# Optimization experiments

Measured on AMD Instinct MI355X. Metric: run time of the kernel, lower is better.

The kernel has to match this reference:

```python
import jax, jax.numpy as jnp
import numpy as np

# Graph / model dims (see shape_source)
N, E = 50000, 1600000          # nodes, edges
NE = 10                         # spectral supports per edge (nfreq)
NIN, NOUT1, NOUT2 = 1, 32, 16   # dataset.num_features, conv out, gate out
NIN2 = NOUT1 + NOUT2            # 48, input to layers 2/3 and fc2


def setup_inputs() -> dict:
    key = jax.random.key(0)
    ks = jax.random.split(key, 32)

    def g(k, shape, scale=0.1):
        return jax.random.normal(k, shape, dtype=jnp.float32) * scale

    inp = {
        "x": g(ks[0], (N, NIN), 1.0),
        "edge_attr": g(ks[1], (E, NE), 1.0),
        "edge_index": jax.random.randint(ks[2], (2, E), 0, N, dtype=jnp.int32),
    }
    i = 3
    for l, nin in zip((1, 2, 3), (NIN, NIN2, NIN2)):
        inp[f"W{l}"] = g(ks[i], (NE, nin, NOUT1)); i += 1   # SpectConv weight [K,in,out]
        inp[f"b{l}"] = g(ks[i], (NOUT1,)); i += 1            # SpectConv bias
        inp[f"U{l}"] = g(ks[i], (nin, NOUT2)); i += 1        # fc11 weight (in,out)
        inp[f"ub{l}"] = g(ks[i], (NOUT2,)); i += 1
        inp[f"V{l}"] = g(ks[i], (nin, NOUT2)); i += 1        # fc12 weight
        inp[f"vb{l}"] = g(ks[i], (NOUT2,)); i += 1
    inp["fc2_w"] = g(ks[i], (NIN2, 1)); i += 1
    inp["fc2_b"] = g(ks[i], (1,))
    return inp


def ml3_layer(x, src, dst, edge_attr, W, b, U, ub, V, vb):
    """ML3Layer(learnedge=False): SpectConv(selfconn=False) + gated linear branch."""
    xs = x[src]  # [E, C] gather source-node features once
    out = jnp.broadcast_to(b, (x.shape[0], W.shape[2]))
    for k in range(W.shape[0]):  # K=10 spectral supports, small fixed loop
        # message: edge_attr[:,k] * x_j ; aggregate: scatter-add at target
        h = jax.ops.segment_sum(edge_attr[:, k:k + 1] * xs, dst, num_segments=x.shape[0])
        out = out + h @ W[k]
    gate = (x @ U + ub) * (x @ V + vb)  # fc11(x) * fc12(x)
    return jnp.concatenate([jax.nn.relu(out), gate], axis=1)  # [N, 48]


def reference(x, edge_attr, W1, b1, U1, ub1, V1, vb1,
              W2, b2, U2, ub2, V2, vb2,
              W3, b3, U3, ub3, V3, vb3,
              fc2_w, fc2_b, edge_index):
    src, dst = edge_index[0], edge_index[1]  # PyG: row 0 = source j, row 1 = target i
    x = ml3_layer(x, src, dst, edge_attr, W1, b1, U1, ub1, V1, vb1)
    x = ml3_layer(x, src, dst, edge_attr, W2, b2, U2, ub2, V2, vb2)
    x = ml3_layer(x, src, dst, edge_attr, W3, b3, U3, ub3, V3, vb3)
    return x @ fc2_w + fc2_b  # [N, 1]
```

## Files before the change

kernel.cpp:

```cpp
#include <hip/hip_runtime.h>


constexpr int K  = 10;
constexpr int C1 = 32;
constexpr int C2 = 16;
constexpr int CC = 48;
constexpr int KD = 480;
constexpr int KSTEPS = 15;
constexpr int RTILE = 4096;
constexpr int RS_WAVES  = 8;
constexpr int RS_ROUNDS = RTILE / (RS_WAVES * 64);

typedef short bf16x8 __attribute__((ext_vector_type(8)));
typedef float f32x4  __attribute__((ext_vector_type(4)));
typedef unsigned int uintx4 __attribute__((ext_vector_type(4)));

static __device__ __forceinline__ unsigned short f2bf(float f) {
    unsigned int u = __float_as_uint(f);
    return (unsigned short)((u + 0x7FFFu + ((u >> 16) & 1u)) >> 16);
}
static __device__ __forceinline__ float bf2f(unsigned short h) {
    return __uint_as_float(((unsigned int)h) << 16);
}
static __device__ __forceinline__ unsigned int pk2(float a, float b) {
    return (unsigned int)f2bf(a) | ((unsigned int)f2bf(b) << 16);
}

__global__ __launch_bounds__(256)
void build_kernel(const float* __restrict__ ea, const int* __restrict__ src,
                  const int* __restrict__ dst, unsigned short* __restrict__ rec,
                  unsigned short* __restrict__ keys0, unsigned int* __restrict__ idx0,
                  int E) {
    int e = blockIdx.x * 256 + threadIdx.x;
    if (e >= E) return;
    keys0[e] = (unsigned short)dst[e];
    idx0[e] = (unsigned int)e;
    const float2* ep = (const float2*)(ea + (size_t)e * K);
    float2 a0 = ep[0], a1 = ep[1], a2 = ep[2], a3 = ep[3], a4 = ep[4];
    uint4 r0, r1;
    r0.x = pk2(a0.x, a0.y); r0.y = pk2(a1.x, a1.y);
    r0.z = pk2(a2.x, a2.y); r0.w = pk2(a3.x, a3.y);
    r1.x = pk2(a4.x, a4.y); r1.y = (unsigned int)src[e];
    r1.z = 0u; r1.w = 0u;
    uint4* rp = (uint4*)(rec + (size_t)e * 16);
    rp[0] = r0; rp[1] = r1;
}

template<int SHIFT>
__global__ __launch_bounds__(256)
void rcount_kernel(const unsigned short* __restrict__ keys,
                   unsigned int* __restrict__ counts, int E, int NB) {
    __shared__ unsigned int h[256];
    h[threadIdx.x] = 0;
    __syncthreads();
    int end = min((blockIdx.x + 1) * RTILE, E);
    for (int i = blockIdx.x * RTILE + threadIdx.x; i < end; i += 256)
        atomicAdd(&h[(keys[i] >> SHIFT) & 255], 1);
    __syncthreads();
    counts[(size_t)threadIdx.x * NB + blockIdx.x] = h[threadIdx.x];
}

__global__ __launch_bounds__(256)
void digit_scan_kernel(const unsigned int* __restrict__ counts,
                       unsigned int* __restrict__ gscan,
                       unsigned int* __restrict__ dtot, int NB) {
    __shared__ unsigned int s[256];
    int d = blockIdx.x, t = threadIdx.x;
    const unsigned int* row = counts + (size_t)d * NB;
    unsigned int* orow = gscan + (size_t)d * NB;
    unsigned int running = 0;
    for (int base = 0; base < NB; base += 256) {
        int i = base + t;
        unsigned int v = (i < NB) ? row[i] : 0u;
        s[t] = v;
        __syncthreads();
#pragma unroll
        for (int off = 1; off < 256; off <<= 1) {
            unsigned int a = (t >= off) ? s[t - off] : 0u;
            __syncthreads();
            s[t] += a;
            __syncthreads();
        }
        if (i < NB) orow[i] = running + s[t] - v;
        running += s[255];
        __syncthreads();
    }
    if (t == 0) dtot[d] = running;
}

template<int SHIFT>
__global__ __launch_bounds__(512)
void rscatter_kernel(const unsigned short* __restrict__ keyIn,
                     const unsigned int* __restrict__ idxIn,
                     const unsigned int* __restrict__ gscan,
                     const unsigned int* __restrict__ dtot,
                     unsigned short* __restrict__ keyOut,
                     unsigned int* __restrict__ idxOut, int E, int NB) {
    __shared__ unsigned int hw[RS_WAVES][256];
    __shared__ unsigned int wex[RS_WAVES][256];
    __shared__ unsigned int wrun[RS_WAVES][256];
    __shared__ unsigned int dbt[256];
    __shared__ unsigned int gb[256];
    int t = threadIdx.x, b = blockIdx.x;
    int w = t >> 6, lane = t & 63;
    {
        unsigned int* hwf = &hw[0][0];
        unsigned int* wrf = &wrun[0][0];
        for (int i = t; i < RS_WAVES * 256; i += 512) { hwf[i] = 0; wrf[i] = 0; }
    }
    unsigned int dv = (t < 256) ? dtot[t] : 0u;
    if (t < 256) dbt[t] = dv;
    __syncthreads();
#pragma unroll
    for (int off = 1; off < 256; off <<= 1) {
        unsigned int a = (t >= off && t < 256) ? dbt[t - off] : 0u;
        __syncthreads();
        if (t < 256) dbt[t] += a;
        __syncthreads();
    }
    if (t < 256) gb[t] = (dbt[t] - dv) + gscan[(size_t)t * NB + b];
    int base = b * RTILE + w * (RTILE / RS_WAVES);
    unsigned short keys[RS_ROUNDS]; unsigned int idxs[RS_ROUNDS]; unsigned int dig[RS_ROUNDS];
#pragma unroll
    for (int r = 0; r < RS_ROUNDS; ++r) {
        int i = base + r * 64 + lane;
        if (i < E) {
            keys[r] = keyIn[i];
            idxs[r] = idxIn[i];
            dig[r] = (keys[r] >> SHIFT) & 255u;
            atomicAdd(&hw[w][dig[r]], 1u);
        } else dig[r] = 0xFFFFFFFFu;
    }
    __syncthreads();
    if (t < 256) {
        unsigned int s = 0;
#pragma unroll
        for (int ww = 0; ww < RS_WAVES; ++ww) { wex[ww][t] = s; s += hw[ww][t]; }
    }
    __syncthreads();
#pragma unroll
    for (int r = 0; r < RS_ROUNDS; ++r) {
        bool valid = dig[r] != 0xFFFFFFFFu;
        unsigned int d = valid ? dig[r] : 0u;
        unsigned long long mask = __ballot(valid);
#pragma unroll
        for (int bit = 0; bit < 8; ++bit) {
            unsigned long long bb = __ballot(valid && ((d >> bit) & 1u));
            mask &= ((d >> bit) & 1u) ? bb : ~bb;
        }
        unsigned int old = 0;
        if (valid) {
            int leader = __ffsll((long long)mask) - 1;
            if (lane == leader) {
                old = wrun[w][d];
                wrun[w][d] = old + (unsigned int)__popcll(mask);
            }
            old = __shfl(old, leader);
            unsigned int myrank = (unsigned int)__popcll(mask & ((1ull << lane) - 1ull));
            unsigned int pos = gb[d] + wex[w][d] + old + myrank;
            keyOut[pos] = keys[r];
            idxOut[pos] = idxs[r];
        }
    }
}

__global__ __launch_bounds__(256)
void materialize_kernel(const unsigned int* __restrict__ idxS,
                        const unsigned short* __restrict__ rec,
                        unsigned short* __restrict__ ea_t,
                        int* __restrict__ src_d, int E, int Epad) {
    int r = blockIdx.x * 256 + threadIdx.x;
    if (r >= Epad) return;
    if (r < E) {
        unsigned int p = idxS[r];
        const uint4* rp = (const uint4*)(rec + (size_t)p * 16);
        uint4 r0 = rp[0], r1 = rp[1];
        src_d[r] = (int)r1.y;
        ea_t[(size_t)0 * Epad + r] = (unsigned short)r0.x;
        ea_t[(size_t)1 * Epad + r] = (unsigned short)(r0.x >> 16);
        ea_t[(size_t)2 * Epad + r] = (unsigned short)r0.y;
        ea_t[(size_t)3 * Epad + r] = (unsigned short)(r0.y >> 16);
        ea_t[(size_t)4 * Epad + r] = (unsigned short)r0.z;
        ea_t[(size_t)5 * Epad + r] = (unsigned short)(r0.z >> 16);
        ea_t[(size_t)6 * Epad + r] = (unsigned short)r0.w;
        ea_t[(size_t)7 * Epad + r] = (unsigned short)(r0.w >> 16);
        ea_t[(size_t)8 * Epad + r] = (unsigned short)r1.x;
        ea_t[(size_t)9 * Epad + r] = (unsigned short)(r1.x >> 16);
    } else {
        src_d[r] = 0;
#pragma unroll
        for (int k = 0; k < K; ++k) ea_t[(size_t)k * Epad + r] = 0;
    }
}

__global__ __launch_bounds__(256)
void rowptr_kernel(const unsigned short* __restrict__ keysS,
                   int* __restrict__ rowptr, int N, int E) {
    int n = blockIdx.x * 256 + threadIdx.x;
    if (n >= N) return;
    int lo = 0, hi = E;
    while (lo < hi) {
        int mid = (lo + hi) >> 1;
        if ((int)keysS[mid] < n) lo = mid + 1; else hi = mid;
    }
    rowptr[n] = lo;
}

static __device__ __forceinline__
void wconv_entry(const float* __restrict__ W, unsigned short* __restrict__ out,
                 int li, int kdact, int cin) {
    int t = li >> 7, rem = li & 127, h = rem >> 6, l = rem & 63;
    int cp = (l & 15) + 16 * h;
    int kbase = t * 32 + ((l >> 4) << 3);
    unsigned int pk[4];
#pragma unroll
    for (int q = 0; q < 4; ++q) {
        unsigned int a = 0, b = 0;
        int kd0 = kbase + 2 * q, kd1 = kd0 + 1;
        if (kd0 < kdact) { int c = kd0 / K, k = kd0 % K; a = f2bf(W[((size_t)k * cin + c) * C1 + cp]); }
        if (kd1 < kdact) { int c = kd1 / K, k = kd1 % K; b = f2bf(W[((size_t)k * cin + c) * C1 + cp]); }
        pk[q] = a | (b << 16);
    }
    uint4 u; u.x = pk[0]; u.y = pk[1]; u.z = pk[2]; u.w = pk[3];
    *(uint4*)(out + (size_t)li * 8) = u;
}

__global__ __launch_bounds__(256)
void wconv_all_kernel(const float* __restrict__ W1, const float* __restrict__ W2,
                      const float* __restrict__ W3,
                      unsigned short* __restrict__ Bfrg1,
                      unsigned short* __restrict__ Bfrag2,
                      unsigned short* __restrict__ Bfrag3) {
    int i = blockIdx.x * 256 + threadIdx.x;
    if (i < 1920)        wconv_entry(W2, Bfrag2, i, KD, CC);
    else if (i < 3840)   wconv_entry(W3, Bfrag3, i - 1920, KD, CC);
    else if (i < 3968)   wconv_entry(W1, Bfrg1, i - 3840, K, 1);
}

__global__ __launch_bounds__(256)
void gather1_kernel(const float* __restrict__ x, const unsigned short* __restrict__ ea_t,
                    const int* __restrict__ src_d, const int* __restrict__ rowptr,
                    unsigned short* __restrict__ Hb, int N, int E, int Epad) {
    int n = blockIdx.x * 4 + (int)(threadIdx.x >> 6);
    if (n >= N) return;
    int l = threadIdx.x & 63;
    int k = l & 15, g = l >> 4;
    int lo = rowptr[n], hi = (n + 1 < N) ? rowptr[n + 1] : E;
    float h = 0.f;
    for (int base = (lo & ~31); base < hi; base += 32) {
        float xs = 0.f;
        int e = base + l;
        if (l < 32 && e >= lo && e < hi) xs = x[src_d[e]];
        bf16x8 av = {0, 0, 0, 0, 0, 0, 0, 0};
        if (k < K) av = *(const bf16x8*)(ea_t + (size_t)k * Epad + base + g * 8);
        float p = 0.f;
#pragma unroll
        for (int j = 0; j < 8; ++j) {
            float xv = __shfl(xs, g * 8 + j);
            p = fmaf(bf2f((unsigned short)av[j]), xv, p);
        }
        h += p;
    }
    h += __shfl_xor(h, 16);
    h += __shfl_xor(h, 32);
    if (l < 32) Hb[(size_t)n * 32 + l] = (l < K) ? f2bf(h) : (unsigned short)0;
}

__global__ __launch_bounds__(256)
void gatherM_kernel(const unsigned short* __restrict__ xb,
                    const unsigned short* __restrict__ ea_t,
                    const int* __restrict__ src_d, const int* __restrict__ rowptr,
                    unsigned short* __restrict__ Hb, int N, int E, int Epad) {
    int n = blockIdx.x * 4 + (int)(threadIdx.x >> 6);
    if (n >= N) return;
    int l = threadIdx.x & 63;
    int lo = rowptr[n], hi = (n + 1 < N) ? rowptr[n + 1] : E;
    int row = l & 15;
    int eoff = (l >> 4) * 8;
    const unsigned short* aplane = ea_t + (size_t)row * Epad;
    f32x4 d0 = {0.f,0.f,0.f,0.f}, d1 = {0.f,0.f,0.f,0.f}, d2 = {0.f,0.f,0.f,0.f};
    for (int base = (lo & ~31); base < hi; base += 32) {
        int e0 = base + eoff;
        uintx4 afu = {0u, 0u, 0u, 0u};
        if (row < K) afu = *(const uintx4*)(aplane + e0);
        int4 sA = *(const int4*)(src_d + e0);
        int4 sB = *(const int4*)(src_d + e0 + 4);
        int s0 = sA.x, s1 = sA.y, s2 = sA.z, s3 = sA.w;
        int s4 = sB.x, s5 = sB.y, s6 = sB.z, s7 = sB.w;
        bool v0,v1,v2,v3,v4,v5,v6,v7;
#define VCK(r, sv, vv) { int e = e0 + r; vv = (e >= lo) && (e < hi); sv = vv ? sv : 0; }
        VCK(0,s0,v0) VCK(1,s1,v1) VCK(2,s2,v2) VCK(3,s3,v3)
        VCK(4,s4,v4) VCK(5,s5,v5) VCK(6,s6,v6) VCK(7,s7,v7)
#undef VCK
        afu[0] &= (v0 ? 0x0000ffffu : 0u) | (v1 ? 0xffff0000u : 0u);
        afu[1] &= (v2 ? 0x0000ffffu : 0u) | (v3 ? 0xffff0000u : 0u);
        afu[2] &= (v4 ? 0x0000ffffu : 0u) | (v5 ? 0xffff0000u : 0u);
        afu[3] &= (v6 ? 0x0000ffffu : 0u) | (v7 ? 0xffff0000u : 0u);
        bf16x8 af = __builtin_bit_cast(bf16x8, afu);
        unsigned int bw0[4], bw1[4], bw2[4];
#define GPAIR(q, sa, sb) { \
        const unsigned short* pa = xb + (size_t)sa * CC + row; \
        const unsigned short* pb = xb + (size_t)sb * CC + row; \
        bw0[q] = (unsigned int)pa[0]  | ((unsigned int)pb[0]  << 16); \
        bw1[q] = (unsigned int)pa[16] | ((unsigned int)pb[16] << 16); \
        bw2[q] = (unsigned int)pa[32] | ((unsigned int)pb[32] << 16); }
        GPAIR(0, s0, s1)
        GPAIR(1, s2, s3)
        GPAIR(2, s4, s5)
        GPAIR(3, s6, s7)
#undef GPAIR
        uintx4 u0 = {bw0[0], bw0[1], bw0[2], bw0[3]};
        uintx4 u1 = {bw1[0], bw1[1], bw1[2], bw1[3]};
        uintx4 u2 = {bw2[0], bw2[1], bw2[2], bw2[3]};
        d0 = __builtin_amdgcn_mfma_f32_16x16x32_bf16(af, __builtin_bit_cast(bf16x8, u0), d0, 0, 0, 0);
        d1 = __builtin_amdgcn_mfma_f32_16x16x32_bf16(af, __builtin_bit_cast(bf16x8, u1), d1, 0, 0, 0);
        d2 = __builtin_amdgcn_mfma_f32_16x16x32_bf16(af, __builtin_bit_cast(bf16x8, u2), d2, 0, 0, 0);
    }
    int rb = (l >> 4) * 4;
    if (rb < K) {
#define STORE_CG(dv, cg) { \
        size_t off = (size_t)n * KD + (size_t)((cg) * 16 + row) * K + rb; \
        *(unsigned int*)(Hb + off) = (unsigned int)f2bf(dv[0]) | ((unsigned int)f2bf(dv[1]) << 16); \
        if (rb != 8) \
            *(unsigned int*)(Hb + off + 2) = (unsigned int)f2bf(dv[2]) | ((unsigned int)f2bf(dv[3]) << 16); }
        STORE_CG(d0, 0) STORE_CG(d1, 1) STORE_CG(d2, 2)
#undef STORE_CG
    }
}

template<int KS>
__global__ __launch_bounds__(256)
void hgemm_kernel(const unsigned short* __restrict__ Hb,
                  const unsigned short* __restrict__ Bfrag,
                  float* __restrict__ acc, int N) {
    __shared__ unsigned short Bl[KS * 2 * 64 * 8];
    for (int i = threadIdx.x; i < KS * 2 * 64 * 4; i += 256)
        ((unsigned int*)Bl)[i] = ((const unsigned int*)Bfrag)[i];
    __syncthreads();
    int tile = blockIdx.x * 4 + (int)(threadIdx.x >> 6);
    int l = threadIdx.x & 63;
    int node0 = tile * 16;
    if (node0 >= N) return;
    constexpr int KDl = KS * 32;
    int row = l & 15, koff = (l >> 4) * 8;
    f32x4 a0 = {0.f,0.f,0.f,0.f}, a1 = {0.f,0.f,0.f,0.f};
#pragma unroll
    for (int t = 0; t < KS; ++t) {
        bf16x8 af = *(const bf16x8*)(Hb + (size_t)(node0 + row) * KDl + t * 32 + koff);
        bf16x8 b0 = *(const bf16x8*)(&Bl[(t * 2 + 0) * 64 * 8 + l * 8]);
        bf16x8 b1 = *(const bf16x8*)(&Bl[(t * 2 + 1) * 64 * 8 + l * 8]);
        a0 = __builtin_amdgcn_mfma_f32_16x16x32_bf16(af, b0, a0, 0, 0, 0);
        a1 = __builtin_amdgcn_mfma_f32_16x16x32_bf16(af, b1, a1, 0, 0, 0);
    }
    int col = l & 15, rbase = (l >> 4) * 4;
#pragma unroll
    for (int r = 0; r < 4; ++r) {
        int node = node0 + rbase + r;
        acc[(size_t)node * C1 + col]      = a0[r];
        acc[(size_t)node * C1 + 16 + col] = a1[r];
    }
}

template<int CIN, bool FINAL>
__global__ __launch_bounds__(256)
void epilogue_kernel(const float* __restrict__ acc, const float* __restrict__ b,
                     const float* __restrict__ x, const float* __restrict__ U,
                     const float* __restrict__ ub, const float* __restrict__ V,
                     const float* __restrict__ vb, float* __restrict__ xnext,
                     unsigned short* __restrict__ xbnext,
                     const float* __restrict__ fc2w, const float* __restrict__ fc2b,
                     float* __restrict__ out, int N) {
    int node = blockIdx.x * 16 + (int)(threadIdx.x >> 4);
    int cp   = threadIdx.x & 15;
    if (node >= N) return;
    float r0 = acc[(size_t)node * C1 + cp]      + b[cp];
    float r1 = acc[(size_t)node * C1 + 16 + cp] + b[16 + cp];
    r0 = r0 > 0.f ? r0 : 0.f;
    r1 = r1 > 0.f ? r1 : 0.f;
    float u = ub[cp], v = vb[cp];
#pragma unroll
    for (int c = 0; c < CIN; ++c) {
        float xc = x[(size_t)node * CIN + c];
        u = fmaf(xc, U[c * C2 + cp], u);
        v = fmaf(xc, V[c * C2 + cp], v);
    }
    float g = u * v;
    if (!FINAL) {
        xnext[(size_t)node * CC + cp]      = r0;
        xnext[(size_t)node * CC + 16 + cp] = r1;
        xnext[(size_t)node * CC + 32 + cp] = g;
        xbnext[(size_t)node * CC + cp]      = f2bf(r0);
        xbnext[(size_t)node * CC + 16 + cp] = f2bf(r1);
        xbnext[(size_t)node * CC + 32 + cp] = f2bf(g);
    } else {
        float dp = r0 * fc2w[cp] + r1 * fc2w[16 + cp] + g * fc2w[32 + cp];
#pragma unroll
        for (int off = 8; off; off >>= 1) dp += __shfl_xor(dp, off, 16);
        if (cp == 0) out[node] = dp + fc2b[0];
    }
}

__global__ __launch_bounds__(256)
void edge1_kernel(const float* __restrict__ x, const float* __restrict__ W1,
                  const float* __restrict__ ea, const int* __restrict__ src,
                  const int* __restrict__ dst, float* __restrict__ acc, int E) {
    __shared__ float Ws[K * C1];
    for (int i = threadIdx.x; i < K * C1; i += 256) Ws[i] = W1[i];
    __syncthreads();
    int gid = blockIdx.x * 256 + threadIdx.x;
    int e = gid >> 5;
    if (e >= E) return;
    int cp = threadIdx.x & 31;
    float xv = x[src[e]];
    const float* eap = ea + (size_t)e * K;
    float m = 0.f;
#pragma unroll
    for (int k = 0; k < K; ++k) m = fmaf(eap[k], Ws[k * C1 + cp], m);
    atomicAdd(acc + (size_t)dst[e] * C1 + cp, m * xv);
}

template<int CIN>
__global__ __launch_bounds__(256)
void xw_kernel(const float* __restrict__ x, const float* __restrict__ W,
               float* __restrict__ XW, int N) {
    __shared__ float Ws[K * CIN * C1];
    for (int i = threadIdx.x; i < K * CIN * C1; i += 256) Ws[i] = W[i];
    __syncthreads();
    int node = blockIdx.x * 8 + (int)(threadIdx.x >> 5);
    int cp = threadIdx.x & 31;
    if (node >= N) return;
    float xv[CIN];
#pragma unroll
    for (int c = 0; c < CIN; ++c) xv[c] = x[(size_t)node * CIN + c];
#pragma unroll
    for (int k = 0; k < K; ++k) {
        float a = 0.f;
#pragma unroll
        for (int c = 0; c < CIN; ++c) a = fmaf(xv[c], Ws[(k * CIN + c) * C1 + cp], a);
        XW[(size_t)node * (K * C1) + k * C1 + cp] = a;
    }
}

__global__ __launch_bounds__(256)
void edge_kernel(const float* __restrict__ XW, const float* __restrict__ ea,
                 const int* __restrict__ src, const int* __restrict__ dst,
                 float* __restrict__ acc, int E) {
    int gid = blockIdx.x * 256 + threadIdx.x;
    int e = gid >> 5;
    if (e >= E) return;
    int cp = threadIdx.x & 31;
    const float* xw = XW + (size_t)src[e] * (K * C1) + cp;
    const float* eap = ea + (size_t)e * K;
    float m = 0.f;
#pragma unroll
    for (int k = 0; k < K; ++k) m = fmaf(eap[k], xw[k * C1], m);
    atomicAdd(acc + (size_t)dst[e] * C1 + cp, m);
}

extern "C" void kernel_launch(void* const* d_in, const int* in_sizes, int n_in,
                              void* d_out, int out_size, void* d_ws, size_t ws_size,
                              hipStream_t stream) {
    const float* x  = (const float*)d_in[0];
    const float* ea = (const float*)d_in[1];
    const int*   ei = (const int*)d_in[2];
    const int N = in_sizes[0];
    const int E = in_sizes[1] / K;
    const int Epad = ((E + 31) & ~31) + 32;
    const int NB = (E + RTILE - 1) / RTILE;
    const int* srcp = ei;
    const int* dstp = ei + E;

    const float *W1 = (const float*)d_in[3],  *b1 = (const float*)d_in[4];
    const float *U1 = (const float*)d_in[5],  *ub1 = (const float*)d_in[6];
    const float *V1 = (const float*)d_in[7],  *vb1 = (const float*)d_in[8];
    const float *W2 = (const float*)d_in[9],  *b2 = (const float*)d_in[10];
    const float *U2 = (const float*)d_in[11], *ub2 = (const float*)d_in[12];
    const float *V2 = (const float*)d_in[13], *vb2 = (const float*)d_in[14];
    const float *W3 = (const float*)d_in[15], *b3 = (const float*)d_in[16];
    const float *U3 = (const float*)d_in[17], *ub3 = (const float*)d_in[18];
    const float *V3 = (const float*)d_in[19], *vb3 = (const float*)d_in[20];
    const float *fc2w = (const float*)d_in[21], *fc2b = (const float*)d_in[22];

    unsigned short* rec   = (unsigned short*)d_ws;
    unsigned short* keys0 = rec + (size_t)E * 16;
    unsigned int*   idx0  = (unsigned int*)(keys0 + Epad);
    unsigned short* keys1 = (unsigned short*)(idx0 + Epad);
    unsigned int*   idx1  = (unsigned int*)(keys1 + Epad);
    unsigned int*   counts = idx1 + Epad;
    unsigned int*   gscan  = counts + (size_t)256 * NB;
    unsigned int*   dtot   = gscan + (size_t)256 * NB;
    unsigned short* ea_t   = (unsigned short*)(dtot + 256);
    int* src_d  = (int*)(ea_t + (size_t)K * Epad);
    int* rowptr = src_d + Epad;
    float* acc  = (float*)(rowptr + N);
    unsigned short* Hb     = (unsigned short*)(acc + (size_t)N * C1);
    unsigned short* Bfrg1  = Hb + (size_t)N * KD;
    unsigned short* Bfrag2 = Bfrg1 + 2 * 64 * 8;
    unsigned short* Bfrag3 = Bfrag2 + KSTEPS * 2 * 64 * 8;
    size_t needMain = (size_t)((char*)(Bfrag3 + KSTEPS * 2 * 64 * 8) - (char*)d_ws);
    float* x2 = (float*)rec;
    float* x3 = x2 + (size_t)N * CC;
    unsigned short* xb2 = (unsigned short*)(x3 + (size_t)N * CC);
    unsigned short* xb3 = xb2 + (size_t)N * CC;
    bool mainPath = (ws_size >= needMain) && (N <= 65536) &&
                    ((size_t)N * CC * 4 * 2 + (size_t)N * CC * 2 * 2 <= (size_t)E * 16 * 2);

    const int eBlocks  = (E + 255) / 256;
    const int epadBlk  = (Epad + 255) / 256;
    const int nwBlocks = (N + 3) / 4;
    const int tiles    = (N + 15) / 16;
    const int gmBlocks = (tiles + 3) / 4;
    const int epBlocks = (N + 15) / 16;

    if (mainPath) {
        build_kernel<<<eBlocks, 256, 0, stream>>>(ea, srcp, dstp, rec, keys0, idx0, E);
        rcount_kernel<0><<<NB, 256, 0, stream>>>(keys0, counts, E, NB);
        digit_scan_kernel<<<256, 256, 0, stream>>>(counts, gscan, dtot, NB);
        rscatter_kernel<0><<<NB, 512, 0, stream>>>(keys0, idx0, gscan, dtot, keys1, idx1, E, NB);
        rcount_kernel<8><<<NB, 256, 0, stream>>>(keys1, counts, E, NB);
        digit_scan_kernel<<<256, 256, 0, stream>>>(counts, gscan, dtot, NB);
        rscatter_kernel<8><<<NB, 512, 0, stream>>>(keys1, idx1, gscan, dtot, keys0, idx0, E, NB);
        materialize_kernel<<<epadBlk, 256, 0, stream>>>(idx0, rec, ea_t, src_d, E, Epad);
        rowptr_kernel<<<(N + 255) / 256, 256, 0, stream>>>(keys0, rowptr, N, E);
        wconv_all_kernel<<<16, 256, 0, stream>>>(W1, W2, W3, Bfrg1, Bfrag2, Bfrag3);

        gather1_kernel<<<nwBlocks, 256, 0, stream>>>(x, ea_t, src_d, rowptr, Hb, N, E, Epad);
        hgemm_kernel<1><<<gmBlocks, 256, 0, stream>>>(Hb, Bfrg1, acc, N);
        epilogue_kernel<1, false><<<epBlocks, 256, 0, stream>>>(
            acc, b1, x, U1, ub1, V1, vb1, x2, xb2, nullptr, nullptr, nullptr, N);

        gatherM_kernel<<<nwBlocks, 256, 0, stream>>>(xb2, ea_t, src_d, rowptr, Hb, N, E, Epad);
        hgemm_kernel<KSTEPS><<<gmBlocks, 256, 0, stream>>>(Hb, Bfrag2, acc, N);
        epilogue_kernel<CC, false><<<epBlocks, 256, 0, stream>>>(
            acc, b2, x2, U2, ub2, V2, vb2, x3, xb3, nullptr, nullptr, nullptr, N);

        gatherM_kernel<<<nwBlocks, 256, 0, stream>>>(xb3, ea_t, src_d, rowptr, Hb, N, E, Epad);
        hgemm_kernel<KSTEPS><<<gmBlocks, 256, 0, stream>>>(Hb, Bfrag3, acc, N);
        epilogue_kernel<CC, true><<<epBlocks, 256, 0, stream>>>(
            acc, b3, x3, U3, ub3, V3, vb3, nullptr, nullptr, fc2w, fc2b, (float*)d_out, N);
    } else {
        float* accF = (float*)d_ws;
        float* x2F  = accF + (size_t)N * C1;
        float* x3F  = x2F + (size_t)N * CC;
        unsigned short* xb2F = (unsigned short*)(x3F + (size_t)N * CC);
        unsigned short* xb3F = xb2F + (size_t)N * CC;
        float* XW = (float*)(xb3F + (size_t)N * CC);
        const int egBlocks = (int)(((size_t)E * 32 + 255) / 256);
        const int xwBlocks = (N + 7) / 8;
        const size_t accBytes = (size_t)N * C1 * sizeof(float);

        hipMemsetAsync(accF, 0, accBytes, stream);
        edge1_kernel<<<egBlocks, 256, 0, stream>>>(x, W1, ea, srcp, dstp, accF, E);
        epilogue_kernel<1, false><<<epBlocks, 256, 0, stream>>>(
            accF, b1, x, U1, ub1, V1, vb1, x2F, xb2F, nullptr, nullptr, nullptr, N);

        hipMemsetAsync(accF, 0, accBytes, stream);
        xw_kernel<CC><<<xwBlocks, 256, 0, stream>>>(x2F, W2, XW, N);
        edge_kernel<<<egBlocks, 256, 0, stream>>>(XW, ea, srcp, dstp, accF, E);
        epilogue_kernel<CC, false><<<epBlocks, 256, 0, stream>>>(
            accF, b2, x2F, U2, ub2, V2, vb2, x3F, xb3F, nullptr, nullptr, nullptr, N);

        hipMemsetAsync(accF, 0, accBytes, stream);
        xw_kernel<CC><<<xwBlocks, 256, 0, stream>>>(x3F, W3, XW, N);
        edge_kernel<<<egBlocks, 256, 0, stream>>>(XW, ea, srcp, dstp, accF, E);
        epilogue_kernel<CC, true><<<epBlocks, 256, 0, stream>>>(
            accF, b3, x3F, U3, ub3, V3, vb3, nullptr, nullptr, fc2w, fc2b, (float*)d_out, N);
    }
}
```

Before: 308.7 us.

## Fuse layer 2/3 edge gather with H×W GEMM via shared-memory tile

Merges the per-node MFMA gather and the follow-up H·W GEMM for layers 2 and 3 into one kernel. Each block gathers 16 nodes (4 per wave) into a padded LDS tile, then two waves multiply it by the weight fragments and write the accumulator directly. This removes the global round-trip of the 50000×480 bf16 H buffer and one launch per layer. In exchange, each wave processes 4 nodes serially, only 2 of 4 waves do the GEMM, and B is read from global memory without LDS staging.

```diff
diff --git a/kernel.cpp b/kernel.cpp
--- a/kernel.cpp
+++ b/kernel.cpp
@@ -7,6 +7,7 @@
 constexpr int CC = 48;
 constexpr int KD = 480;
 constexpr int KSTEPS = 15;
+constexpr int HROW = 488;
 constexpr int RTILE = 4096;
 constexpr int RS_WAVES  = 8;
 constexpr int RS_ROUNDS = RTILE / (RS_WAVES * 64);
@@ -267,64 +268,91 @@
 }
 
 __global__ __launch_bounds__(256)
-void gatherM_kernel(const unsigned short* __restrict__ xb,
-                    const unsigned short* __restrict__ ea_t,
-                    const int* __restrict__ src_d, const int* __restrict__ rowptr,
-                    unsigned short* __restrict__ Hb, int N, int E, int Epad) {
-    int n = blockIdx.x * 4 + (int)(threadIdx.x >> 6);
-    if (n >= N) return;
-    int l = threadIdx.x & 63;
-    int lo = rowptr[n], hi = (n + 1 < N) ? rowptr[n + 1] : E;
+void fusedM_kernel(const unsigned short* __restrict__ xb,
+                   const unsigned short* __restrict__ ea_t,
+                   const int* __restrict__ src_d, const int* __restrict__ rowptr,
+                   const unsigned short* __restrict__ Bfrag,
+                   float* __restrict__ acc, int N, int E, int Epad) {
+    __shared__ unsigned short Hs[16][HROW];
+    int node0 = blockIdx.x * 16;
+    if (node0 >= N) return;
+    int t = threadIdx.x;
+    int w = t >> 6, l = t & 63;
     int row = l & 15;
     int eoff = (l >> 4) * 8;
     const unsigned short* aplane = ea_t + (size_t)row * Epad;
-    f32x4 d0 = {0.f,0.f,0.f,0.f}, d1 = {0.f,0.f,0.f,0.f}, d2 = {0.f,0.f,0.f,0.f};
-    for (int base = (lo & ~31); base < hi; base += 32) {
-        int e0 = base + eoff;
-        uintx4 afu = {0u, 0u, 0u, 0u};
-        if (row < K) afu = *(const uintx4*)(aplane + e0);
-        int4 sA = *(const int4*)(src_d + e0);
-        int4 sB = *(const int4*)(src_d + e0 + 4);
-        int s0 = sA.x, s1 = sA.y, s2 = sA.z, s3 = sA.w;
-        int s4 = sB.x, s5 = sB.y, s6 = sB.z, s7 = sB.w;
-        bool v0,v1,v2,v3,v4,v5,v6,v7;
+#pragma unroll
+    for (int q = 0; q < 4; ++q) {
+        int hrow = w * 4 + q;
+        int n = node0 + hrow;
+        f32x4 d0 = {0.f,0.f,0.f,0.f}, d1 = {0.f,0.f,0.f,0.f}, d2 = {0.f,0.f,0.f,0.f};
+        if (n < N) {
+            int lo = rowptr[n], hi = (n + 1 < N) ? rowptr[n + 1] : E;
+            for (int base = (lo & ~31); base < hi; base += 32) {
+                int e0 = base + eoff;
+                uintx4 afu = {0u, 0u, 0u, 0u};
+                if (row < K) afu = *(const uintx4*)(aplane + e0);
+                int4 sA = *(const int4*)(src_d + e0);
+                int4 sB = *(const int4*)(src_d + e0 + 4);
+                int s0 = sA.x, s1 = sA.y, s2 = sA.z, s3 = sA.w;
+                int s4 = sB.x, s5 = sB.y, s6 = sB.z, s7 = sB.w;
+                bool v0,v1,v2,v3,v4,v5,v6,v7;
 #define VCK(r, sv, vv) { int e = e0 + r; vv = (e >= lo) && (e < hi); sv = vv ? sv : 0; }
-        VCK(0,s0,v0) VCK(1,s1,v1) VCK(2,s2,v2) VCK(3,s3,v3)
-        VCK(4,s4,v4) VCK(5,s5,v5) VCK(6,s6,v6) VCK(7,s7,v7)
+                VCK(0,s0,v0) VCK(1,s1,v1) VCK(2,s2,v2) VCK(3,s3,v3)
+                VCK(4,s4,v4) VCK(5,s5,v5) VCK(6,s6,v6) VCK(7,s7,v7)
 #undef VCK
-        afu[0] &= (v0 ? 0x0000ffffu : 0u) | (v1 ? 0xffff0000u : 0u);
-        afu[1] &= (v2 ? 0x0000ffffu : 0u) | (v3 ? 0xffff0000u : 0u);
-        afu[2] &= (v4 ? 0x0000ffffu : 0u) | (v5 ? 0xffff0000u : 0u);
-        afu[3] &= (v6 ? 0x0000ffffu : 0u) | (v7 ? 0xffff0000u : 0u);
-        bf16x8 af = __builtin_bit_cast(bf16x8, afu);
-        unsigned int bw0[4], bw1[4], bw2[4];
-#define GPAIR(q, sa, sb) { \
-        const unsigned short* pa = xb + (size_t)sa * CC + row; \
-        const unsigned short* pb = xb + (size_t)sb * CC + row; \
-        bw0[q] = (unsigned int)pa[0]  | ((unsigned int)pb[0]  << 16); \
-        bw1[q] = (unsigned int)pa[16] | ((unsigned int)pb[16] << 16); \
-        bw2[q] = (unsigned int)pa[32] | ((unsigned int)pb[32] << 16); }
-        GPAIR(0, s0, s1)
-        GPAIR(1, s2, s3)
-        GPAIR(2, s4, s5)
-        GPAIR(3, s6, s7)
+                afu[0] &= (v0 ? 0x0000ffffu : 0u) | (v1 ? 0xffff0000u : 0u);
+                afu[1] &= (v2 ? 0x0000ffffu : 0u) | (v3 ? 0xffff0000u : 0u);
+                afu[2] &= (v4 ? 0x0000ffffu : 0u) | (v5 ? 0xffff0000u : 0u);
+                afu[3] &= (v6 ? 0x0000ffffu : 0u) | (v7 ? 0xffff0000u : 0u);
+                bf16x8 af = __builtin_bit_cast(bf16x8, afu);
+                unsigned int bw0[4], bw1[4], bw2[4];
+#define GPAIR(q2, sa, sb) { \
+                const unsigned short* pa = xb + (size_t)sa * CC + row; \
+                const unsigned short* pb = xb + (size_t)sb * CC + row; \
+                bw0[q2] = (unsigned int)pa[0]  | ((unsigned int)pb[0]  << 16); \
+                bw1[q2] = (unsigned int)pa[16] | ((unsigned int)pb[16] << 16); \
+                bw2[q2] = (unsigned int)pa[32] | ((unsigned int)pb[32] << 16); }
+                GPAIR(0, s0, s1)
+                GPAIR(1, s2, s3)
+                GPAIR(2, s4, s5)
+                GPAIR(3, s6, s7)
 #undef GPAIR
-        uintx4 u0 = {bw0[0], bw0[1], bw0[2], bw0[3]};
-        uintx4 u1 = {bw1[0], bw1[1], bw1[2], bw1[3]};
-        uintx4 u2 = {bw2[0], bw2[1], bw2[2], bw2[3]};
-        d0 = __builtin_amdgcn_mfma_f32_16x16x32_bf16(af, __builtin_bit_cast(bf16x8, u0), d0, 0, 0, 0);
-        d1 = __builtin_amdgcn_mfma_f32_16x16x32_bf16(af, __builtin_bit_cast(bf16x8, u1), d1, 0, 0, 0);
-        d2 = __builtin_amdgcn_mfma_f32_16x16x32_bf16(af, __builtin_bit_cast(bf16x8, u2), d2, 0, 0, 0);
-    }
-    int rb = (l >> 4) * 4;
-    if (rb < K) {
+                uintx4 u0 = {bw0[0], bw0[1], bw0[2], bw0[3]};
+                uintx4 u1 = {bw1[0], bw1[1], bw1[2], bw1[3]};
+                uintx4 u2 = {bw2[0], bw2[1], bw2[2], bw2[3]};
+                d0 = __builtin_amdgcn_mfma_f32_16x16x32_bf16(af, __builtin_bit_cast(bf16x8, u0), d0, 0, 0, 0);
+                d1 = __builtin_amdgcn_mfma_f32_16x16x32_bf16(af, __builtin_bit_cast(bf16x8, u1), d1, 0, 0, 0);
+                d2 = __builtin_amdgcn_mfma_f32_16x16x32_bf16(af, __builtin_bit_cast(bf16x8, u2), d2, 0, 0, 0);
+            }
+        }
+        int rb = (l >> 4) * 4;
+        if (rb < K) {
 #define STORE_CG(dv, cg) { \
-        size_t off = (size_t)n * KD + (size_t)((cg) * 16 + row) * K + rb; \
-        *(unsigned int*)(Hb + off) = (unsigned int)f2bf(dv[0]) | ((unsigned int)f2bf(dv[1]) << 16); \
-        if (rb != 8) \
-            *(unsigned int*)(Hb + off + 2) = (unsigned int)f2bf(dv[2]) | ((unsigned int)f2bf(dv[3]) << 16); }
-        STORE_CG(d0, 0) STORE_CG(d1, 1) STORE_CG(d2, 2)
+            int off = ((cg) * 16 + row) * K + rb; \
+            *(unsigned int*)(&Hs[hrow][off]) = (unsigned int)f2bf(dv[0]) | ((unsigned int)f2bf(dv[1]) << 16); \
+            if (rb != 8) \
+                *(unsigned int*)(&Hs[hrow][off + 2]) = (unsigned int)f2bf(dv[2]) | ((unsigned int)f2bf(dv[3]) << 16); }
+            STORE_CG(d0, 0) STORE_CG(d1, 1) STORE_CG(d2, 2)
 #undef STORE_CG
+        }
+    }
+    __syncthreads();
+    if (w < 2) {
+        int koff2 = (l >> 4) * 8;
+        f32x4 a = {0.f, 0.f, 0.f, 0.f};
+#pragma unroll
+        for (int ts = 0; ts < KSTEPS; ++ts) {
+            bf16x8 af = *(const bf16x8*)(&Hs[row][ts * 32 + koff2]);
+            bf16x8 b  = *(const bf16x8*)(Bfrag + (size_t)(ts * 2 + w) * 512 + l * 8);
+            a = __builtin_amdgcn_mfma_f32_16x16x32_bf16(af, b, a, 0, 0, 0);
+        }
+        int col = l & 15, rbase = (l >> 4) * 4;
+#pragma unroll
+        for (int r = 0; r < 4; ++r) {
+            int node = node0 + rbase + r;
+            if (node < N) acc[(size_t)node * C1 + w * 16 + col] = a[r];
+        }
     }
 }
 
@@ -529,13 +557,11 @@
         epilogue_kernel<1, false><<<epBlocks, 256, 0, stream>>>(
             acc, b1, x, U1, ub1, V1, vb1, x2, xb2, nullptr, nullptr, nullptr, N);
 
-        gatherM_kernel<<<nwBlocks, 256, 0, stream>>>(xb2, ea_t, src_d, rowptr, Hb, N, E, Epad);
-        hgemm_kernel<KSTEPS><<<gmBlocks, 256, 0, stream>>>(Hb, Bfrag2, acc, N);
+        fusedM_kernel<<<tiles, 256, 0, stream>>>(xb2, ea_t, src_d, rowptr, Bfrag2, acc, N, E, Epad);
         epilogue_kernel<CC, false><<<epBlocks, 256, 0, stream>>>(
             acc, b2, x2, U2, ub2, V2, vb2, x3, xb3, nullptr, nullptr, nullptr, N);
 
-        gatherM_kernel<<<nwBlocks, 256, 0, stream>>>(xb3, ea_t, src_d, rowptr, Hb, N, E, Epad);
-        hgemm_kernel<KSTEPS><<<gmBlocks, 256, 0, stream>>>(Hb, Bfrag3, acc, N);
+        fusedM_kernel<<<tiles, 256, 0, stream>>>(xb3, ea_t, src_d, rowptr, Bfrag3, acc, N, E, Epad);
         epilogue_kernel<CC, true><<<epBlocks, 256, 0, stream>>>(
             acc, b3, x3, U3, ub3, V3, vb3, nullptr, nullptr, fc2w, fc2b, (float*)d_out, N);
     } else {
```

Measured after the change: 288.4 us. 6.6% less time.
